# Kernel optimization log

Hardware: AMD Instinct MI355X
Metric: run time of the kernel (lower is better)

The kernel has to match this reference:

```python
import jax, jax.numpy as jnp
import numpy as np

IMG_SHAPE = (256, 256, 256)


def _rot3(a):
    # Rx @ Ry @ Rz, matching _compute_rotation
    ax, ay, az = a[0], a[1], a[2]
    cx, sx = jnp.cos(ax), jnp.sin(ax)
    cy, sy = jnp.cos(ay), jnp.sin(ay)
    cz, sz = jnp.cos(az), jnp.sin(az)
    one = jnp.ones_like(ax)
    zero = jnp.zeros_like(ax)
    Rx = jnp.stack([jnp.stack([one, zero, zero]),
                    jnp.stack([zero, cx, -sx]),
                    jnp.stack([zero, sx, cx])])
    Ry = jnp.stack([jnp.stack([cy, zero, sy]),
                    jnp.stack([zero, one, zero]),
                    jnp.stack([-sy, zero, cy])])
    Rz = jnp.stack([jnp.stack([cz, -sz, zero]),
                    jnp.stack([sz, cz, zero]),
                    jnp.stack([zero, zero, one])])
    return Rx @ Ry @ Rz


def _rigid4(a, t, cog):
    # T_center_inv @ T_trans @ T_rot @ T_center
    R = _rot3(a)
    Tc = jnp.eye(4, dtype=a.dtype).at[:3, 3].set(-cog)
    Tci = jnp.eye(4, dtype=a.dtype).at[:3, 3].set(cog)
    Tt = jnp.eye(4, dtype=a.dtype).at[:3, 3].set(t)
    Tr = jnp.eye(4, dtype=a.dtype).at[:3, :3].set(R)
    return Tci @ Tt @ Tr @ Tc


def _trilinear(vol, di, dj, dk):
    # fast_3D_interp_torch(mode='linear'): trilinear interp, zero outside bounds
    D, H, W = vol.shape
    ok = (di >= 0) & (di <= D - 1) & (dj >= 0) & (dj <= H - 1) & (dk >= 0) & (dk <= W - 1)
    di = jnp.clip(di, 0.0, D - 1)
    dj = jnp.clip(dj, 0.0, H - 1)
    dk = jnp.clip(dk, 0.0, W - 1)
    fi = jnp.floor(di).astype(jnp.int32)
    fj = jnp.floor(dj).astype(jnp.int32)
    fk = jnp.floor(dk).astype(jnp.int32)
    ci = jnp.clip(fi + 1, 0, D - 1)
    cj = jnp.clip(fj + 1, 0, H - 1)
    ck = jnp.clip(fk + 1, 0, W - 1)
    wi = di - fi
    wj = dj - fj
    wk = dk - fk
    out = (vol[fi, fj, fk] * (1 - wi) * (1 - wj) * (1 - wk)
           + vol[fi, fj, ck] * (1 - wi) * (1 - wj) * wk
           + vol[fi, cj, fk] * (1 - wi) * wj * (1 - wk)
           + vol[fi, cj, ck] * (1 - wi) * wj * wk
           + vol[ci, fj, fk] * wi * (1 - wj) * (1 - wk)
           + vol[ci, fj, ck] * wi * (1 - wj) * wk
           + vol[ci, cj, fk] * wi * wj * (1 - wk)
           + vol[ci, cj, ck] * wi * wj * wk)
    return jnp.where(ok, out, jnp.zeros_like(out))


def setup_inputs() -> dict:
    key = jax.random.key(0)
    k1, k2 = jax.random.split(key)
    image_targ = jax.random.normal(k1, (1, 1) + IMG_SHAPE, dtype=jnp.float32)
    # small rotation so most of the warped grid stays in bounds (angle_factor=1)
    angle = 0.1 * jax.random.normal(k2, (1, 3), dtype=jnp.float32)
    translation = jnp.zeros((1, 3), dtype=jnp.float32)
    v2r = np.eye(4, dtype=np.float32)
    v2r[:3, 3] = -127.5  # center-of-volume RAS origin
    ref_v2r = jnp.asarray(v2r)
    flo_v2r = jnp.asarray(v2r)
    cog = jnp.zeros((3,), dtype=jnp.float32)
    return {"image_targ": image_targ, "angle": angle, "translation": translation,
            "ref_v2r": ref_v2r, "flo_v2r": flo_v2r, "cog": cog}


def reference(image_targ, angle, translation, ref_v2r, flo_v2r, cog):
    # tx_factor = angle_factor = 1 -> params used as-is
    T_rig = jax.vmap(lambda a, t: _rigid4(a, t, cog))(angle, translation)  # [B,4,4]
    T = (jnp.linalg.inv(flo_v2r) @ T_rig[0] @ ref_v2r).astype(jnp.float32)
    D, H, W = image_targ.shape[2:]
    gi, gj, gk = jnp.meshgrid(jnp.arange(D, dtype=jnp.float32),
                              jnp.arange(H, dtype=jnp.float32),
                              jnp.arange(W, dtype=jnp.float32), indexing='ij')
    di = T[0, 0] * gi + T[0, 1] * gj + T[0, 2] * gk + T[0, 3]
    dj = T[1, 0] * gi + T[1, 1] * gj + T[1, 2] * gk + T[1, 3]
    dk = T[2, 0] * gi + T[2, 1] * gj + T[2, 2] * gk + T[2, 3]
    image_reg = _trilinear(image_targ[0, 0], di, dj, dk)
    return image_reg[None, None]
```

## Files before the change

### kernel.cpp

```cpp
#include <hip/hip_runtime.h>
#include <math.h>

#define DD 256
#define HH 256
#define WW 256
#define IPT 8

typedef float f2v __attribute__((ext_vector_type(2)));
typedef f2v __attribute__((aligned(4))) f2u;

__global__ void compute_T_kernel(const float* __restrict__ angle,
                                 const float* __restrict__ trans,
                                 const float* __restrict__ ref_v2r,
                                 const float* __restrict__ flo_v2r,
                                 const float* __restrict__ cog,
                                 float* __restrict__ Tout ) {
    if (blockIdx.x != 0 || threadIdx.x != 0) return;

    const float ax = angle[0], ay = angle[1], az = angle[2];
    const float cx = cosf(ax), sx = sinf(ax);
    const float cy = cosf(ay), sy = sinf(ay);
    const float cz = cosf(az), sz = sinf(az);

    float R[3][3];
    const float a00 = cy,       a01 = 0.0f, a02 = sy;
    const float a10 = sx * sy,  a11 = cx,   a12 = -sx * cy;
    const float a20 = -cx * sy, a21 = sx,   a22 = cx * cy;
    R[0][0] = a00 * cz + a01 * sz; R[0][1] = -a00 * sz + a01 * cz; R[0][2] = a02;
    R[1][0] = a10 * cz + a11 * sz; R[1][1] = -a10 * sz + a11 * cz; R[1][2] = a12;
    R[2][0] = a20 * cz + a21 * sz; R[2][1] = -a20 * sz + a21 * cz; R[2][2] = a22;

    float Trig[4][4];
    for (int r = 0; r < 4; ++r)
        for (int c = 0; c < 4; ++c)
            Trig[r][c] = (r == c) ? 1.0f : 0.0f;
    for (int r = 0; r < 3; ++r) {
        for (int c = 0; c < 3; ++c) Trig[r][c] = R[r][c];
        Trig[r][3] = cog[r] + trans[r]
                   - (R[r][0] * cog[0] + R[r][1] * cog[1] + R[r][2] * cog[2]);
    }

    float m[16], inv[16];
    for (int q = 0; q < 16; ++q) m[q] = flo_v2r[q];
    inv[0]  =  m[5]*m[10]*m[15] - m[5]*m[11]*m[14] - m[9]*m[6]*m[15]
             + m[9]*m[7]*m[14] + m[13]*m[6]*m[11] - m[13]*m[7]*m[10];
    inv[4]  = -m[4]*m[10]*m[15] + m[4]*m[11]*m[14] + m[8]*m[6]*m[15]
             - m[8]*m[7]*m[14] - m[12]*m[6]*m[11] + m[12]*m[7]*m[10];
    inv[8]  =  m[4]*m[9]*m[15] - m[4]*m[11]*m[13] - m[8]*m[5]*m[15]
             + m[8]*m[7]*m[13] + m[12]*m[5]*m[11] - m[12]*m[7]*m[9];
    inv[12] = -m[4]*m[9]*m[14] + m[4]*m[10]*m[13] + m[8]*m[5]*m[14]
             - m[8]*m[6]*m[13] - m[12]*m[5]*m[10] + m[12]*m[6]*m[9];
    inv[1]  = -m[1]*m[10]*m[15] + m[1]*m[11]*m[14] + m[9]*m[2]*m[15]
             - m[9]*m[3]*m[14] - m[13]*m[2]*m[11] + m[13]*m[3]*m[10];
    inv[5]  =  m[0]*m[10]*m[15] - m[0]*m[11]*m[14] - m[8]*m[2]*m[15]
             + m[8]*m[3]*m[14] + m[12]*m[2]*m[11] - m[12]*m[3]*m[10];
    inv[9]  = -m[0]*m[9]*m[15] + m[0]*m[11]*m[13] + m[8]*m[1]*m[15]
             - m[8]*m[3]*m[13] - m[12]*m[1]*m[11] + m[12]*m[3]*m[9];
    inv[13] =  m[0]*m[9]*m[14] - m[0]*m[10]*m[13] - m[8]*m[1]*m[14]
             + m[8]*m[2]*m[13] + m[12]*m[1]*m[10] - m[12]*m[2]*m[9];
    inv[2]  =  m[1]*m[6]*m[15] - m[1]*m[7]*m[14] - m[5]*m[2]*m[15]
             + m[5]*m[3]*m[14] + m[13]*m[2]*m[7] - m[13]*m[3]*m[6];
    inv[6]  = -m[0]*m[6]*m[15] + m[0]*m[7]*m[14] + m[4]*m[2]*m[15]
             - m[4]*m[3]*m[14] - m[12]*m[2]*m[7] + m[12]*m[3]*m[6];
    inv[10] =  m[0]*m[5]*m[15] - m[0]*m[7]*m[13] - m[4]*m[1]*m[15]
             + m[4]*m[3]*m[13] + m[12]*m[1]*m[7] - m[12]*m[3]*m[5];
    inv[14] = -m[0]*m[5]*m[14] + m[0]*m[6]*m[13] + m[4]*m[1]*m[14]
             - m[4]*m[2]*m[13] - m[12]*m[1]*m[6] + m[12]*m[2]*m[5];
    inv[3]  = -m[1]*m[6]*m[11] + m[1]*m[7]*m[10] + m[5]*m[2]*m[11]
             - m[5]*m[3]*m[10] - m[9]*m[2]*m[7] + m[9]*m[3]*m[6];
    inv[7]  =  m[0]*m[6]*m[11] - m[0]*m[7]*m[10] - m[4]*m[2]*m[11]
             + m[4]*m[3]*m[10] + m[8]*m[2]*m[7] - m[8]*m[3]*m[6];
    inv[11] = -m[0]*m[5]*m[11] + m[0]*m[7]*m[9] + m[4]*m[1]*m[11]
             - m[4]*m[3]*m[9] - m[8]*m[1]*m[7] + m[8]*m[3]*m[5];
    inv[15] =  m[0]*m[5]*m[10] - m[0]*m[6]*m[9] - m[4]*m[1]*m[10]
             + m[4]*m[2]*m[9] + m[8]*m[1]*m[6] - m[8]*m[2]*m[5];
    const float det = m[0]*inv[0] + m[1]*inv[4] + m[2]*inv[8] + m[3]*inv[12];
    const float rdet = 1.0f / det;

    float M1[4][4];
    for (int r = 0; r < 4; ++r)
        for (int c = 0; c < 4; ++c) {
            float s = 0.0f;
            for (int q = 0; q < 4; ++q) s += Trig[r][q] * ref_v2r[q * 4 + c];
            M1[r][c] = s;
        }
    for (int r = 0; r < 3; ++r)
        for (int c = 0; c < 4; ++c) {
            float s = 0.0f;
            for (int q = 0; q < 4; ++q) s += (inv[r * 4 + q] * rdet) * M1[q][c];
            Tout[r * 4 + c] = s;
        }
}

__global__ __launch_bounds__(256) void warp_kernel(
        const float* __restrict__ vol,
        const float* __restrict__ T,
        float* __restrict__ out) {
    const float t0 = T[0],  t1 = T[1],  t2  = T[2],  t3  = T[3];
    const float t4 = T[4],  t5 = T[5],  t6  = T[6],  t7  = T[7];
    const float t8 = T[8],  t9 = T[9],  t10 = T[10], t11 = T[11];

    const int bid = blockIdx.x;
    const int xcd = bid & 7;
    const int n = bid >> 3;
    const int bi = (xcd >> 2) & 1;
    const int bj = (xcd >> 1) & 1;
    const int bk = xcd & 1;
    const int kt = n & 1;
    const int jt = (n >> 1) & 31;
    const int it = n >> 6;

    const int tx = threadIdx.x & 63;
    const int ty = threadIdx.x >> 6;

    const int i0 = (bi << 7) + it * IPT;
    const int j  = (bj << 7) + (jt << 2) + ty;
    const int k  = (bk << 7) + (kt << 6) + tx;

    const float gj = (float)j, gk = (float)k;
    const float di0 = t0 * (float)i0 + t1 * gj + t2  * gk + t3;
    const float dj0 = t4 * (float)i0 + t5 * gj + t6  * gk + t7;
    const float dk0 = t8 * (float)i0 + t9 * gj + t10 * gk + t11;

    f2v vv[IPT][4];
    {
        float di = di0, dj = dj0, dk = dk0;
#pragma unroll
        for (int s = 0; s < IPT; ++s) {
            const float cdi = fminf(fmaxf(di, 0.0f), (float)(DD - 1));
            const float cdj = fminf(fmaxf(dj, 0.0f), (float)(HH - 1));
            const float cdk = fminf(fmaxf(dk, 0.0f), (float)(WW - 1));

            const int fi = (int)cdi;
            const int fj = (int)cdj;
            const int fk = (int)cdk;
            const int ci = min(fi + 1, DD - 1);
            const int cj = min(fj + 1, HH - 1);
            const int pk = min(fk, WW - 2);

            const int fi_o = fi << 16, ci_o = ci << 16;
            const int fj_o = fj << 8,  cj_o = cj << 8;

            vv[s][0] = *(const f2u*)(vol + (fi_o + fj_o + pk));
            vv[s][1] = *(const f2u*)(vol + (fi_o + cj_o + pk));
            vv[s][2] = *(const f2u*)(vol + (ci_o + fj_o + pk));
            vv[s][3] = *(const f2u*)(vol + (ci_o + cj_o + pk));

            di += t0; dj += t4; dk += t8;
        }
    }

    const int out_base = (i0 << 16) + (j << 8) + k;
    {
        float di = di0, dj = dj0, dk = dk0;
#pragma unroll
        for (int s = 0; s < IPT; ++s) {
            const bool ok = (di >= 0.0f) & (di <= (float)(DD - 1)) &
                            (dj >= 0.0f) & (dj <= (float)(HH - 1)) &
                            (dk >= 0.0f) & (dk <= (float)(WW - 1));

            const float cdi = fminf(fmaxf(di, 0.0f), (float)(DD - 1));
            const float cdj = fminf(fmaxf(dj, 0.0f), (float)(HH - 1));
            const float cdk = fminf(fmaxf(dk, 0.0f), (float)(WW - 1));

            const int fi = (int)cdi;
            const int fj = (int)cdj;
            const int fk = (int)cdk;

            const float wi = cdi - (float)fi;
            const float wj = cdj - (float)fj;
            const float wk = cdk - (float)fk;

            const bool hi = (fk == (WW - 1));
            const float v000 = hi ? vv[s][0].y : vv[s][0].x;
            const float v001 = vv[s][0].y;
            const float v010 = hi ? vv[s][1].y : vv[s][1].x;
            const float v011 = vv[s][1].y;
            const float v100 = hi ? vv[s][2].y : vv[s][2].x;
            const float v101 = vv[s][2].y;
            const float v110 = hi ? vv[s][3].y : vv[s][3].x;
            const float v111 = vv[s][3].y;

            const float c00 = v000 + (v001 - v000) * wk;
            const float c01 = v010 + (v011 - v010) * wk;
            const float c10 = v100 + (v101 - v100) * wk;
            const float c11 = v110 + (v111 - v110) * wk;
            const float c0  = c00 + (c01 - c00) * wj;
            const float c1  = c10 + (c11 - c10) * wj;
            const float val = c0 + (c1 - c0) * wi;

            __builtin_nontemporal_store(ok ? val : 0.0f,
                                        &out[out_base + (s << 16)]);

            di += t0; dj += t4; dk += t8;
        }
    }
}

extern "C" void kernel_launch(void* const* d_in, const int* in_sizes, int n_in,
                              void* d_out, int out_size, void* d_ws, size_t ws_size,
                              hipStream_t stream) {
    const float* image_targ  = (const float*)d_in[0];
    const float* angle       = (const float*)d_in[1];
    const float* translation = (const float*)d_in[2];
    const float* ref_v2r     = (const float*)d_in[3];
    const float* flo_v2r     = (const float*)d_in[4];
    const float* cog         = (const float*)d_in[5];
    float* out = (float*)d_out;
    float* Tws = (float*)d_ws;

    compute_T_kernel<<<1, 64, 0, stream>>>(angle, translation, ref_v2r,
                                           flo_v2r, cog, Tws);
    warp_kernel<<<(DD * HH) / IPT, 256, 0, stream>>>(image_targ, Tws, out);
}
```

Measured before the change: 177.1 us.

## Stage rotated source bounding box into LDS per 16^3 output tile

Each block now handles a 16x16x16 output cube. It computes the bounding box of the transformed source coordinates, cooperatively loads that box into shared memory with 16-byte loads, then does the trilinear gathers from LDS. If the box does not fit (more than 16384 floats or wider than 32 in k), it falls back to direct global gathers. The aim is to replace scattered global gather traffic with coalesced tile loads and LDS reuse, at the cost of a 64KB LDS footprint that limits occupancy, a sync, and possible LDS bank conflicts. The output store pattern changes to 16-wide k rows, giving shorter contiguous writes.

```diff
diff --git a/kernel.cpp b/kernel.cpp
--- a/kernel.cpp
+++ b/kernel.cpp
@@ -4,10 +4,13 @@
 #define DD 256
 #define HH 256
 #define WW 256
-#define IPT 8
+#define TS 16
+#define LDSF 16384
 
 typedef float f2v __attribute__((ext_vector_type(2)));
 typedef f2v __attribute__((aligned(4))) f2u;
+typedef float f4v __attribute__((ext_vector_type(4)));
+typedef f4v __attribute__((aligned(4))) f4u;
 
 __global__ void compute_T_kernel(const float* __restrict__ angle,
                                  const float* __restrict__ trans,
@@ -106,93 +109,168 @@
     const int bi = (xcd >> 2) & 1;
     const int bj = (xcd >> 1) & 1;
     const int bk = xcd & 1;
-    const int kt = n & 1;
-    const int jt = (n >> 1) & 31;
+    const int kt = n & 7;
+    const int jt = (n >> 3) & 7;
     const int it = n >> 6;
 
-    const int tx = threadIdx.x & 63;
-    const int ty = threadIdx.x >> 6;
-
-    const int i0 = (bi << 7) + it * IPT;
-    const int j  = (bj << 7) + (jt << 2) + ty;
-    const int k  = (bk << 7) + (kt << 6) + tx;
-
+    const int i0 = (bi << 7) + (it << 4);
+    const int j0 = (bj << 7) + (jt << 4);
+    const int k0 = (bk << 7) + (kt << 4);
+
+    const int tid = threadIdx.x;
+    const int kl = tid & 15;
+    const int jl = tid >> 4;
+    const int j = j0 + jl;
+    const int k = k0 + kl;
     const float gj = (float)j, gk = (float)k;
-    const float di0 = t0 * (float)i0 + t1 * gj + t2  * gk + t3;
-    const float dj0 = t4 * (float)i0 + t5 * gj + t6  * gk + t7;
-    const float dk0 = t8 * (float)i0 + t9 * gj + t10 * gk + t11;
-
-    f2v vv[IPT][4];
-    {
-        float di = di0, dj = dj0, dk = dk0;
-#pragma unroll
-        for (int s = 0; s < IPT; ++s) {
-            const float cdi = fminf(fmaxf(di, 0.0f), (float)(DD - 1));
-            const float cdj = fminf(fmaxf(dj, 0.0f), (float)(HH - 1));
-            const float cdk = fminf(fmaxf(dk, 0.0f), (float)(WW - 1));
-
-            const int fi = (int)cdi;
-            const int fj = (int)cdj;
-            const int fk = (int)cdk;
-            const int ci = min(fi + 1, DD - 1);
-            const int cj = min(fj + 1, HH - 1);
-            const int pk = min(fk, WW - 2);
-
-            const int fi_o = fi << 16, ci_o = ci << 16;
-            const int fj_o = fj << 8,  cj_o = cj << 8;
-
-            vv[s][0] = *(const f2u*)(vol + (fi_o + fj_o + pk));
-            vv[s][1] = *(const f2u*)(vol + (fi_o + cj_o + pk));
-            vv[s][2] = *(const f2u*)(vol + (ci_o + fj_o + pk));
-            vv[s][3] = *(const f2u*)(vol + (ci_o + cj_o + pk));
-
-            di += t0; dj += t4; dk += t8;
-        }
+    const int out_base = (i0 << 16) + (j << 8) + k;
+
+    __shared__ float sv[LDSF];
+
+    float mni =  1e30f, mxi = -1e30f;
+    float mnj =  1e30f, mxj = -1e30f;
+    float mnk =  1e30f, mxk = -1e30f;
+#pragma unroll
+    for (int c = 0; c < 8; ++c) {
+        const float ci_ = (float)(i0 + ((c & 1) ? (TS - 1) : 0));
+        const float cj_ = (float)(j0 + ((c & 2) ? (TS - 1) : 0));
+        const float ck_ = (float)(k0 + ((c & 4) ? (TS - 1) : 0));
+        const float di = t0 * ci_ + t1 * cj_ + t2  * ck_ + t3;
+        const float dj = t4 * ci_ + t5 * cj_ + t6  * ck_ + t7;
+        const float dk = t8 * ci_ + t9 * cj_ + t10 * ck_ + t11;
+        mni = fminf(mni, di); mxi = fmaxf(mxi, di);
+        mnj = fminf(mnj, dj); mxj = fmaxf(mxj, dj);
+        mnk = fminf(mnk, dk); mxk = fmaxf(mxk, dk);
     }
-
-    const int out_base = (i0 << 16) + (j << 8) + k;
-    {
-        float di = di0, dj = dj0, dk = dk0;
-#pragma unroll
-        for (int s = 0; s < IPT; ++s) {
-            const bool ok = (di >= 0.0f) & (di <= (float)(DD - 1)) &
-                            (dj >= 0.0f) & (dj <= (float)(HH - 1)) &
-                            (dk >= 0.0f) & (dk <= (float)(WW - 1));
-
-            const float cdi = fminf(fmaxf(di, 0.0f), (float)(DD - 1));
-            const float cdj = fminf(fmaxf(dj, 0.0f), (float)(HH - 1));
-            const float cdk = fminf(fmaxf(dk, 0.0f), (float)(WW - 1));
-
-            const int fi = (int)cdi;
-            const int fj = (int)cdj;
-            const int fk = (int)cdk;
-
-            const float wi = cdi - (float)fi;
-            const float wj = cdj - (float)fj;
-            const float wk = cdk - (float)fk;
-
-            const bool hi = (fk == (WW - 1));
-            const float v000 = hi ? vv[s][0].y : vv[s][0].x;
-            const float v001 = vv[s][0].y;
-            const float v010 = hi ? vv[s][1].y : vv[s][1].x;
-            const float v011 = vv[s][1].y;
-            const float v100 = hi ? vv[s][2].y : vv[s][2].x;
-            const float v101 = vv[s][2].y;
-            const float v110 = hi ? vv[s][3].y : vv[s][3].x;
-            const float v111 = vv[s][3].y;
-
-            const float c00 = v000 + (v001 - v000) * wk;
-            const float c01 = v010 + (v011 - v010) * wk;
-            const float c10 = v100 + (v101 - v100) * wk;
-            const float c11 = v110 + (v111 - v110) * wk;
-            const float c0  = c00 + (c01 - c00) * wj;
-            const float c1  = c10 + (c11 - c10) * wj;
-            const float val = c0 + (c1 - c0) * wi;
-
-            __builtin_nontemporal_store(ok ? val : 0.0f,
-                                        &out[out_base + (s << 16)]);
-
-            di += t0; dj += t4; dk += t8;
+    int lo_i = (int)fminf(fmaxf(mni, 0.0f), 255.0f);
+    int hi_i = (int)fminf(fmaxf(mxi, 0.0f), 255.0f);
+    int lo_j = (int)fminf(fmaxf(mnj, 0.0f), 255.0f);
+    int hi_j = (int)fminf(fmaxf(mxj, 0.0f), 255.0f);
+    int lo_k = (int)fminf(fmaxf(mnk, 0.0f), 255.0f);
+    int hi_k = (int)fminf(fmaxf(mxk, 0.0f), 255.0f);
+    lo_i = min(max(lo_i - 1, 0), 252);
+    lo_j = min(max(lo_j - 1, 0), 252);
+    lo_k = min(max(lo_k - 1, 0), 252);
+    hi_i = min(max(hi_i + 2, lo_i + 3), 255);
+    hi_j = min(max(hi_j + 2, lo_j + 3), 255);
+    hi_k = min(max(hi_k + 2, lo_k + 3), 255);
+    const int Si = hi_i - lo_i + 1;
+    const int Sj = hi_j - lo_j + 1;
+    const int Sk = hi_k - lo_k + 1;
+    const int SjSk = Sj * Sk;
+    const bool fits = (Si * SjSk <= LDSF) && (Sk <= 32);
+
+    if (fits) {
+        {
+            const int kk0 = (tid & 7) << 2;
+            const int rj  = tid >> 3;
+            if (rj < Sj && kk0 < Sk) {
+                const int kk = min(kk0, Sk - 4);
+                const float* gp = vol + ((lo_i << 16) + ((lo_j + rj) << 8)
+                                         + lo_k + kk);
+                float* sp = sv + rj * Sk + kk;
+                for (int li = 0; li < Si; ++li, gp += 65536, sp += SjSk) {
+                    const f4v p = *(const f4u*)gp;
+                    *(f4u*)sp = p;
+                }
+            }
+        }
+        __syncthreads();
+
+#pragma unroll
+        for (int IT = 0; IT < 4; ++IT) {
+            const float gi_ = (float)(i0 + IT * 4);
+            float di_ = t0 * gi_ + t1 * gj + t2  * gk + t3;
+            float dj_ = t4 * gi_ + t5 * gj + t6  * gk + t7;
+            float dk_ = t8 * gi_ + t9 * gj + t10 * gk + t11;
+#pragma unroll
+            for (int s_ = 0; s_ < 4; ++s_) {
+                const float cdi = fminf(fmaxf(di_, 0.0f), (float)(DD - 1));
+                const float cdj = fminf(fmaxf(dj_, 0.0f), (float)(HH - 1));
+                const float cdk = fminf(fmaxf(dk_, 0.0f), (float)(WW - 1));
+                const int fi = (int)cdi;
+                const int fj = (int)cdj;
+                const int fk = (int)cdk;
+                const int ci = min(fi + 1, DD - 1);
+                const int cj = min(fj + 1, HH - 1);
+                const int pk = min(fk, WW - 2);
+                const float wi = cdi - (float)fi;
+                const float wj = cdj - (float)fj;
+                const float wk = cdk - (float)pk;
+                const bool ok_ = (di_ >= 0.0f) & (di_ <= (float)(DD - 1)) &
+                                 (dj_ >= 0.0f) & (dj_ <= (float)(HH - 1)) &
+                                 (dk_ >= 0.0f) & (dk_ <= (float)(WW - 1));
+
+                const int o_fi = (fi - lo_i) * SjSk;
+                const int o_ci = (ci - lo_i) * SjSk;
+                const int o_fj = (fj - lo_j) * Sk;
+                const int o_cj = (cj - lo_j) * Sk;
+                const int pl = pk - lo_k;
+
+                const f2v v0 = *(const f2u*)(sv + o_fi + o_fj + pl);
+                const f2v v1 = *(const f2u*)(sv + o_fi + o_cj + pl);
+                const f2v v2 = *(const f2u*)(sv + o_ci + o_fj + pl);
+                const f2v v3 = *(const f2u*)(sv + o_ci + o_cj + pl);
+
+                const float c00 = v0.x + (v0.y - v0.x) * wk;
+                const float c01 = v1.x + (v1.y - v1.x) * wk;
+                const float c10 = v2.x + (v2.y - v2.x) * wk;
+                const float c11 = v3.x + (v3.y - v3.x) * wk;
+                const float c0  = c00 + (c01 - c00) * wj;
+                const float c1  = c10 + (c11 - c10) * wj;
+                const float val = c0 + (c1 - c0) * wi;
+
+                __builtin_nontemporal_store(ok_ ? val : 0.0f,
+                    &out[out_base + ((IT * 4 + s_) << 16)]);
+
+                di_ += t0; dj_ += t4; dk_ += t8;
+            }
+        }
+    } else {
+#pragma unroll
+        for (int IT = 0; IT < 4; ++IT) {
+            const float gi_ = (float)(i0 + IT * 4);
+            float di_ = t0 * gi_ + t1 * gj + t2  * gk + t3;
+            float dj_ = t4 * gi_ + t5 * gj + t6  * gk + t7;
+            float dk_ = t8 * gi_ + t9 * gj + t10 * gk + t11;
+#pragma unroll
+            for (int s_ = 0; s_ < 4; ++s_) {
+                const float cdi = fminf(fmaxf(di_, 0.0f), (float)(DD - 1));
+                const float cdj = fminf(fmaxf(dj_, 0.0f), (float)(HH - 1));
+                const float cdk = fminf(fmaxf(dk_, 0.0f), (float)(WW - 1));
+                const int fi = (int)cdi;
+                const int fj = (int)cdj;
+                const int fk = (int)cdk;
+                const int ci = min(fi + 1, DD - 1);
+                const int cj = min(fj + 1, HH - 1);
+                const int pk = min(fk, WW - 2);
+                const float wi = cdi - (float)fi;
+                const float wj = cdj - (float)fj;
+                const float wk = cdk - (float)pk;
+                const bool ok_ = (di_ >= 0.0f) & (di_ <= (float)(DD - 1)) &
+                                 (dj_ >= 0.0f) & (dj_ <= (float)(HH - 1)) &
+                                 (dk_ >= 0.0f) & (dk_ <= (float)(WW - 1));
+
+                const int fi_o = fi << 16, ci_o = ci << 16;
+                const int fj_o = fj << 8,  cj_o = cj << 8;
+                const f2v v0 = *(const f2u*)(vol + (fi_o + fj_o + pk));
+                const f2v v1 = *(const f2u*)(vol + (fi_o + cj_o + pk));
+                const f2v v2 = *(const f2u*)(vol + (ci_o + fj_o + pk));
+                const f2v v3 = *(const f2u*)(vol + (ci_o + cj_o + pk));
+
+                const float c00 = v0.x + (v0.y - v0.x) * wk;
+                const float c01 = v1.x + (v1.y - v1.x) * wk;
+                const float c10 = v2.x + (v2.y - v2.x) * wk;
+                const float c11 = v3.x + (v3.y - v3.x) * wk;
+                const float c0  = c00 + (c01 - c00) * wj;
+                const float c1  = c10 + (c11 - c10) * wj;
+                const float val = c0 + (c1 - c0) * wi;
+
+                __builtin_nontemporal_store(ok_ ? val : 0.0f,
+                    &out[out_base + ((IT * 4 + s_) << 16)]);
+
+                di_ += t0; dj_ += t4; dk_ += t8;
+            }
         }
     }
 }
@@ -211,5 +289,6 @@
 
     compute_T_kernel<<<1, 64, 0, stream>>>(angle, translation, ref_v2r,
                                            flo_v2r, cog, Tws);
-    warp_kernel<<<(DD * HH) / IPT, 256, 0, stream>>>(image_targ, Tws, out);
+    warp_kernel<<<(DD / TS) * (HH / TS) * (WW / TS), 256, 0, stream>>>(
+        image_targ, Tws, out);
 }
```

Measured after the change: 199.5 us. +12.6%, slower.
